# Optimization experiments

Measured on AMD Instinct MI355X. Metric: run time of the kernel, lower is better.

Reference implementation:

```python
import jax, jax.numpy as jnp
import numpy as np
import math

B = 262144
STATE = 6
TOTAL_MEAS = 27
HID = 256
INPUT_DIM = TOTAL_MEAS * 2 + 1 + STATE + 12  # 73
PI = math.pi
NORM_R_SCALE = 500.0 / 150000.0
ANG_IDX = np.array([0, 1, 3, 4, 6, 9, 10, 12, 13, 15, 18, 19, 21, 22, 24])
ANG_MASK = np.zeros((TOTAL_MEAS,), dtype=bool)
ANG_MASK[ANG_IDX] = True


def setup_inputs() -> dict:
    key = jax.random.key(0)
    ks = jax.random.split(key, 16)
    s = lambda fan: 1.0 / math.sqrt(fan)
    inp = {
        "meas": jax.random.normal(ks[0], (B, TOTAL_MEAS), jnp.float32),
        "mask": jnp.ones((B, TOTAL_MEAS), jnp.float32),
        "dt": jax.random.uniform(ks[1], (B,), jnp.float32),
        "baselines": jax.random.normal(ks[2], (B, 12), jnp.float32),
        "x_prev": jax.random.normal(ks[3], (B, STATE), jnp.float32),
        "hx": jnp.zeros((B, HID), jnp.float32),
        # GRU params (torch gate order: r, z, n)
        "W_ih": jax.random.uniform(ks[4], (3 * HID, INPUT_DIM), jnp.float32, -s(HID), s(HID)),
        "W_hh": jax.random.uniform(ks[5], (3 * HID, HID), jnp.float32, -s(HID), s(HID)),
        "b_ih": jax.random.uniform(ks[6], (3 * HID,), jnp.float32, -s(HID), s(HID)),
        "b_hh": jax.random.uniform(ks[7], (3 * HID,), jnp.float32, -s(HID), s(HID)),
        # LayerNorm
        "ln_g": jnp.ones((HID,), jnp.float32),
        "ln_b": jnp.zeros((HID,), jnp.float32),
        # MLP head: 256 -> 256 -> 128 -> 6*27
        "W1": jax.random.uniform(ks[8], (256, HID), jnp.float32, -s(HID), s(HID)),
        "b1": jax.random.uniform(ks[9], (256,), jnp.float32, -s(HID), s(HID)),
        "W2": jax.random.uniform(ks[10], (128, 256), jnp.float32, -s(256), s(256)),
        "b2": jax.random.uniform(ks[11], (128,), jnp.float32, -s(256), s(256)),
        "W3": jax.random.uniform(ks[12], (STATE * TOTAL_MEAS, 128), jnp.float32, -s(128), s(128)),
        "b3": jax.random.uniform(ks[13], (STATE * TOTAL_MEAS,), jnp.float32, -s(128), s(128)),
    }
    return inp


def _wrap_angle(a):
    two_pi = 2.0 * PI
    return a - two_pi * jnp.round(a / two_pi)


def _platform_y_pred(x_rel):
    # x_rel: [B, 6] -> [B, 9] radar/EO measurement
    r_xy = jnp.sqrt(x_rel[:, 0] ** 2 + x_rel[:, 2] ** 2 + 1e-9)
    az = jnp.arctan2(x_rel[:, 2], x_rel[:, 0]) / PI
    el = jnp.arctan2(x_rel[:, 4], r_xy) / PI
    r = jnp.sqrt(x_rel[:, 0] ** 2 + x_rel[:, 2] ** 2 + x_rel[:, 4] ** 2 + 1e-9)
    z = jnp.zeros_like(r)
    return jnp.stack([az, el, r, az, el, z, az, z, z], axis=1)


def _forward(meas, mask, dt, baselines, x_prev, hx,
             W_ih, W_hh, b_ih, b_hh, ln_g, ln_b, W1, b1, W2, b2, W3, b3):
    # f_predict (CV model): x0 += dt*x1, x2 += dt*x3, x4 += dt*x5
    dt_scaled = dt * NORM_R_SCALE  # [B]
    zcol = jnp.zeros_like(x_prev[:, :1])
    shift = jnp.concatenate([x_prev[:, 1:2], zcol, x_prev[:, 3:4], zcol, x_prev[:, 5:6], zcol], axis=1)
    x_minus = x_prev + dt_scaled[:, None] * shift  # [B, 6]

    y_pred = jnp.concatenate([
        _platform_y_pred(x_minus),
        _platform_y_pred(x_minus - baselines[:, 0:6]),
        _platform_y_pred(x_minus - baselines[:, 6:12]),
    ], axis=1)  # [B, 27]

    innov = meas - y_pred
    wrapped = _wrap_angle(innov * PI) / PI
    innov = jnp.where(jnp.asarray(ANG_MASK)[None, :], wrapped, innov)
    innov = innov * mask

    rnn_in = jnp.concatenate([innov, mask, dt[:, None], x_minus, baselines], axis=1)  # [B, 73]

    # single-step GRU (torch semantics, gate order r,z,n)
    gi = rnn_in @ W_ih.T + b_ih  # [B, 3H]
    gh = hx @ W_hh.T + b_hh      # [B, 3H]
    gi_r, gi_z, gi_n = jnp.split(gi, 3, axis=1)
    gh_r, gh_z, gh_n = jnp.split(gh, 3, axis=1)
    r = jax.nn.sigmoid(gi_r + gh_r)
    z = jax.nn.sigmoid(gi_z + gh_z)
    n = jnp.tanh(gi_n + r * gh_n)
    h_new = (1.0 - z) * n + z * hx  # [B, H]

    # LayerNorm
    mu = jnp.mean(h_new, axis=-1, keepdims=True)
    var = jnp.var(h_new, axis=-1, keepdims=True)
    h_ln = (h_new - mu) / jnp.sqrt(var + 1e-5) * ln_g + ln_b

    # MLP gain head (dropout inactive at inference)
    f1 = jax.nn.relu(h_ln @ W1.T + b1)
    f2 = jax.nn.relu(f1 @ W2.T + b2)
    K = (f2 @ W3.T + b3).reshape(-1, STATE, TOTAL_MEAS)
    K = jnp.clip(K, -3.0, 3.0)

    correction = jnp.einsum('bsm,bm->bs', K, innov)
    x_new = jnp.clip(x_minus + correction, -5.0, 5.0)
    return x_new, h_new


def reference(meas, mask, dt, baselines, x_prev, hx,
              W_ih, W_hh, b_ih, b_hh, ln_g, ln_b, W1, b1, W2, b2, W3, b3):
    return _forward(meas, mask, dt, baselines, x_prev, hx,
                    W_ih, W_hh, b_ih, b_hh, ln_g, ln_b, W1, b1, W2, b2, W3, b3)
```

## Files before the change

### kernel.cpp

```cpp
#include <hip/hip_runtime.h>
#include <math.h>

#define B_TOTAL  262144
#define ROWS     64
#define NWG      (B_TOTAL/ROWS)
#define NTHR     512
#define PI_F     3.14159265358979323846f
#define NORM_R   (500.0f/150000.0f)

typedef float  f32x4  __attribute__((ext_vector_type(4)));
typedef short  bf16x8 __attribute__((ext_vector_type(8)));

#define SRZ 352
#define SNI 96
#define SNH 256
#define SW1 256
#define SW2 256
#define SW3 128
#define OFF_RZ 0
#define OFF_NI (OFF_RZ + 512*SRZ)
#define OFF_NH (OFF_NI + 256*SNI)
#define OFF_W1 (OFF_NH + 256*SNH)
#define OFF_W2 (OFF_W1 + 256*SW1)
#define OFF_W3 (OFF_W2 + 128*SW2)
#define W_TOTAL (OFF_W3 + 256*SW3)

#define RSTRIDE 104
#define LDS_HB   (ROWS*RSTRIDE*2)
#define LDS_F1   (LDS_HB + ROWS*256*2)
#define LDS_STG  (LDS_F1 + ROWS*256*2)
#define LDS_XMC  (LDS_STG + 4*16384)
#define LDS_TOTAL (LDS_XMC + ROWS*6*4)

#define WAIT_VM4 asm volatile("s_waitcnt vmcnt(4)" ::: "memory")
#define WAIT_VM2 asm volatile("s_waitcnt vmcnt(2)" ::: "memory")
#define WAIT_VM0 asm volatile("s_waitcnt vmcnt(0)" ::: "memory")
#define BARv     __builtin_amdgcn_s_barrier()
#define PRE_G(g) do { if ((g) < 47) WAIT_VM4; else if ((g) == 47) WAIT_VM2; else WAIT_VM0; BARv; } while(0)

__device__ __forceinline__ ushort f2bf(float f){
    union { float f; unsigned u; } v; v.f = f;
    unsigned r = v.u + 0x7FFFu + ((v.u >> 16) & 1u);
    return (ushort)(r >> 16);
}
__device__ __forceinline__ float b2f(ushort u){
    union { unsigned u; float f; } v; v.u = ((unsigned)u) << 16;
    return v.f;
}
__device__ __forceinline__ float sigm(float x){ return 1.0f/(1.0f+__expf(-x)); }
__device__ __forceinline__ float tanh_(float x){ return 1.0f - 2.0f/(__expf(2.0f*x)+1.0f); }
__device__ __forceinline__ int swzb(int row, int k){
    return ((row<<9) + (k<<1)) ^ ((row&7)<<4);
}

__device__ __forceinline__ void stageA(const ushort* pb, int stride, int koff,
                                       char* dst, int w, int lane) {
    #pragma unroll
    for (int i = 0; i < 2; ++i) {
        int idx  = (w*2 + i)*64 + lane;
        int col  = idx >> 2;
        int kq   = (idx & 3) ^ ((col >> 1) & 3);
        const ushort* g = pb + (size_t)col*stride + koff + kq*8;
        __builtin_amdgcn_global_load_lds(
            (const __attribute__((address_space(1))) void*)g,
            (__attribute__((address_space(3))) void*)(dst + (w*2+i)*1024),
            16, 0, 0);
    }
}
__device__ __forceinline__ void stageB(const ushort* pb, int stride, int koff,
                                       char* dst, int w, int lane) {
    #pragma unroll
    for (int i = 0; i < 2; ++i) {
        int idx  = (w*2 + i)*64 + lane;
        int col  = idx >> 3;
        int kq   = (idx & 7) ^ (col & 7);
        const ushort* g = pb + (size_t)col*stride + koff + kq*8;
        __builtin_amdgcn_global_load_lds(
            (const __attribute__((address_space(1))) void*)g,
            (__attribute__((address_space(3))) void*)(dst + (w*2+i)*1024),
            16, 0, 0);
    }
}
__device__ __forceinline__ bf16x8 rdA16(const char* sb, int col, int lk){
    int slot = lk ^ ((col >> 1) & 3);
    return *(const bf16x8*)(sb + col*64 + slot*16);
}
__device__ __forceinline__ bf16x8 rdB16(const char* sb, int col, int ksub, int lk){
    int slot = ((ksub<<2)|lk) ^ (col & 7);
    return *(const bf16x8*)(sb + col*128 + slot*16);
}

__global__ void prep_weights(const float* __restrict__ W_ih, const float* __restrict__ W_hh,
                             const float* __restrict__ W1, const float* __restrict__ W2,
                             const float* __restrict__ W3, ushort* __restrict__ ws)
{
    int id = blockIdx.x*256 + threadIdx.x;
    if (id >= W_TOTAL) return;
    float v = 0.0f;
    if (id < OFF_NI) {
        int t = id; int n = t / SRZ, k = t - n*SRZ;
        if (k < 73) v = W_ih[n*73 + k];
        else if (k >= 96) v = W_hh[n*256 + (k-96)];
    } else if (id < OFF_NH) {
        int t = id - OFF_NI; int n = t / SNI, k = t - n*SNI;
        if (k < 73) v = W_ih[(512+n)*73 + k];
    } else if (id < OFF_W1) {
        int t = id - OFF_NH; int n = t >> 8, k = t & 255;
        v = W_hh[(512+n)*256 + k];
    } else if (id < OFF_W2) {
        int t = id - OFF_W1; int n = t >> 8, k = t & 255;
        v = W1[n*256 + k];
    } else if (id < OFF_W3) {
        int t = id - OFF_W2; int n = t >> 8, k = t & 255;
        v = W2[n*256 + k];
    } else {
        int t = id - OFF_W3; int n = t >> 7, k = t & 127;
        if (n < 162) v = W3[n*128 + k];
    }
    ws[id] = f2bf(v);
}

#define MM8(ACC) do { _Pragma("unroll") \
    for (int j = 0; j < 4; ++j) { \
        bf16x8 b = rdA16(sb, nq*64 + j*16 + lr, lk); \
        ACC[0][j] = __builtin_amdgcn_mfma_f32_16x16x32_bf16(a0, b, ACC[0][j], 0,0,0); \
        ACC[1][j] = __builtin_amdgcn_mfma_f32_16x16x32_bf16(a1, b, ACC[1][j], 0,0,0); \
    } } while(0)

__global__ __launch_bounds__(NTHR, 1) void knet_mfma(
    const float* __restrict__ meas, const float* __restrict__ mask,
    const float* __restrict__ dt,   const float* __restrict__ baselines,
    const float* __restrict__ x_prev, const float* __restrict__ hx,
    const float* __restrict__ b_ih, const float* __restrict__ b_hh,
    const float* __restrict__ ln_g, const float* __restrict__ ln_b,
    const float* __restrict__ b1,   const float* __restrict__ b2,
    const float* __restrict__ b3,
    const ushort* __restrict__ ws,
    float* __restrict__ out)
{
    extern __shared__ char smem[];
    ushort* Rb  = (ushort*)smem;
    char*   Hb  = smem + LDS_HB;
    char*   F1  = smem + LDS_F1;
    char*   STG = smem + LDS_STG;
    float*  xmc = (float*)(smem + LDS_XMC);

    const int tid  = threadIdx.x;
    const int w    = __builtin_amdgcn_readfirstlane(tid >> 6);
    const int nq   = w & 3;
    const int mh   = w >> 2;
    const int lane = tid & 63;
    const int lr   = lane & 15;
    const int lk   = lane >> 4;
    const int lk8  = lk * 8;
    const int row0 = blockIdx.x * ROWS;
    const int mrow = mh*32 + lr;
    float* hout = out + (size_t)B_TOTAL*6;

    stageA(ws + OFF_RZ, SRZ, 0*32, STG + (0<<14), w, lane);
    stageA(ws + OFF_RZ, SRZ, 1*32, STG + (1<<14), w, lane);
    stageA(ws + OFF_RZ, SRZ, 2*32, STG + (2<<14), w, lane);

    float* scr = (float*)F1;
    {
        const size_t m0 = (size_t)row0*27;
        for (int i = tid; i < 1728; i += NTHR) scr[i]        = meas[m0 + i];
        for (int i = tid; i < 1728; i += NTHR) scr[1728 + i] = mask[m0 + i];
        const size_t b0 = (size_t)row0*12;
        for (int i = tid; i < 768; i += NTHR)  scr[3456 + i] = baselines[b0 + i];
        if (tid < 384) scr[4224 + tid] = x_prev[(size_t)row0*6 + tid];
        if (tid < 64)  scr[4608 + tid] = dt[row0 + tid];
        const size_t hbase = (size_t)row0 * 256;
        #pragma unroll
        for (int ii = 0; ii < 4; ++ii) {
            int cid = tid + ii*NTHR;
            int r  = cid >> 5;
            int k0 = (cid & 31) << 3;
            const float4* p = (const float4*)(hx + hbase + (size_t)r*256 + k0);
            float4 u = p[0], v2 = p[1];
            bf16x8 o;
            o[0]=(short)f2bf(u.x);  o[1]=(short)f2bf(u.y);  o[2]=(short)f2bf(u.z);  o[3]=(short)f2bf(u.w);
            o[4]=(short)f2bf(v2.x); o[5]=(short)f2bf(v2.y); o[6]=(short)f2bf(v2.z); o[7]=(short)f2bf(v2.w);
            *(bf16x8*)(Hb + swzb(r, k0)) = o;
        }
    }
    __syncthreads();

    if (w < 4) {
        const int row = lane;
        const float dtv = scr[4608 + row];
        const float dts = dtv * NORM_R;
        float xp[6], xm[6];
        #pragma unroll
        for (int s = 0; s < 6; ++s) xp[s] = scr[4224 + row*6 + s];
        xm[0] = xp[0] + dts*xp[1]; xm[1] = xp[1];
        xm[2] = xp[2] + dts*xp[3]; xm[3] = xp[3];
        xm[4] = xp[4] + dts*xp[5]; xm[5] = xp[5];
        if (w < 3) {
            float xr[6];
            #pragma unroll
            for (int s = 0; s < 6; ++s) {
                float b = (w == 0) ? 0.0f : scr[3456 + row*12 + (w-1)*6 + s];
                xr[s] = xm[s] - b;
            }
            float rxy = sqrtf(xr[0]*xr[0] + xr[2]*xr[2] + 1e-9f);
            float azv = atan2f(xr[2], xr[0]) * (1.0f/PI_F);
            float elv = atan2f(xr[4], rxy)   * (1.0f/PI_F);
            float rrv = sqrtf(xr[0]*xr[0] + xr[2]*xr[2] + xr[4]*xr[4] + 1e-9f);
            float y[9] = {azv, elv, rrv, azv, elv, 0.0f, azv, 0.0f, 0.0f};
            const bool ang[9] = {true,true,false,true,true,false,true,false,false};
            #pragma unroll
            for (int i = 0; i < 9; ++i) {
                int m = w*9 + i;
                float ms = scr[1728 + row*27 + m];
                float v  = scr[row*27 + m] - y[i];
                if (ang[i]) v = v - 2.0f*rintf(v*0.5f);
                v *= ms;
                Rb[row*RSTRIDE + m]      = f2bf(v);
                Rb[row*RSTRIDE + 27 + m] = f2bf(ms);
            }
        } else {
            Rb[row*RSTRIDE + 54] = f2bf(dtv);
            #pragma unroll
            for (int s = 0; s < 6; ++s) Rb[row*RSTRIDE + 55 + s] = f2bf(xm[s]);
            #pragma unroll
            for (int q = 0; q < 12; ++q) Rb[row*RSTRIDE + 61 + q] = f2bf(scr[3456 + row*12 + q]);
            #pragma unroll
            for (int k = 73; k < 96; ++k) Rb[row*RSTRIDE + k] = 0;
            #pragma unroll
            for (int s = 0; s < 6; ++s) xmc[row*6 + s] = xm[s];
        }
    }
    __syncthreads();

    f32x4 ar[2][4], az_[2][4], gi_[2][4], gh_[2][4];
    #pragma unroll
    for (int i = 0; i < 2; ++i)
        #pragma unroll
        for (int j = 0; j < 4; ++j) {
            ar[i][j]=(f32x4){0,0,0,0}; az_[i][j]=(f32x4){0,0,0,0};
            gi_[i][j]=(f32x4){0,0,0,0}; gh_[i][j]=(f32x4){0,0,0,0};
        }

    #pragma unroll
    for (int kb = 0; kb < 11; ++kb) {
        PRE_G(kb);
        char* dst = STG + (((kb+3)&3)<<14);
        if (kb < 8) stageA(ws + OFF_RZ, SRZ, (kb+3)*32, dst, w, lane);
        else        stageA(ws + OFF_RZ + (size_t)256*SRZ, SRZ, (kb-8)*32, dst, w, lane);
        const char* sb = STG + ((kb&3)<<14);
        bf16x8 a0, a1;
        if (kb < 3) { a0 = *(const bf16x8*)(Rb + mrow*RSTRIDE + kb*32 + lk8);
                      a1 = *(const bf16x8*)(Rb + (mrow+16)*RSTRIDE + kb*32 + lk8); }
        else        { a0 = *(const bf16x8*)(Hb + swzb(mrow,    (kb-3)*32 + lk8));
                      a1 = *(const bf16x8*)(Hb + swzb(mrow+16, (kb-3)*32 + lk8)); }
        __builtin_amdgcn_s_setprio(1);
        MM8(ar);
        __builtin_amdgcn_s_setprio(0);
    }
    #pragma unroll
    for (int kb = 0; kb < 11; ++kb) {
        PRE_G(11+kb);
        char* dst = STG + (((kb+14)&3)<<14);
        if (kb < 8) stageA(ws + OFF_RZ + (size_t)256*SRZ, SRZ, (kb+3)*32, dst, w, lane);
        else        stageA(ws + OFF_NI, SNI, (kb-8)*32, dst, w, lane);
        const char* sb = STG + (((11+kb)&3)<<14);
        bf16x8 a0, a1;
        if (kb < 3) { a0 = *(const bf16x8*)(Rb + mrow*RSTRIDE + kb*32 + lk8);
                      a1 = *(const bf16x8*)(Rb + (mrow+16)*RSTRIDE + kb*32 + lk8); }
        else        { a0 = *(const bf16x8*)(Hb + swzb(mrow,    (kb-3)*32 + lk8));
                      a1 = *(const bf16x8*)(Hb + swzb(mrow+16, (kb-3)*32 + lk8)); }
        __builtin_amdgcn_s_setprio(1);
        MM8(az_);
        __builtin_amdgcn_s_setprio(0);
    }
    #pragma unroll
    for (int kb = 0; kb < 3; ++kb) {
        PRE_G(22+kb);
        char* dst = STG + (((kb+25)&3)<<14);
        stageA(ws + OFF_NH, SNH, kb*32, dst, w, lane);
        const char* sb = STG + (((22+kb)&3)<<14);
        bf16x8 a0 = *(const bf16x8*)(Rb + mrow*RSTRIDE + kb*32 + lk8);
        bf16x8 a1 = *(const bf16x8*)(Rb + (mrow+16)*RSTRIDE + kb*32 + lk8);
        __builtin_amdgcn_s_setprio(1);
        MM8(gi_);
        __builtin_amdgcn_s_setprio(0);
    }
    #pragma unroll
    for (int kb = 0; kb < 8; ++kb) {
        PRE_G(25+kb);
        char* dst = STG + (((kb+28)&3)<<14);
        if (kb < 5) stageA(ws + OFF_NH, SNH, (kb+3)*32, dst, w, lane);
        else        stageA(ws + OFF_W1, SW1, (kb-5)*32, dst, w, lane);
        const char* sb = STG + (((25+kb)&3)<<14);
        bf16x8 a0 = *(const bf16x8*)(Hb + swzb(mrow,    kb*32 + lk8));
        bf16x8 a1 = *(const bf16x8*)(Hb + swzb(mrow+16, kb*32 + lk8));
        __builtin_amdgcn_s_setprio(1);
        MM8(gh_);
        __builtin_amdgcn_s_setprio(0);
    }
    #pragma unroll
    for (int j = 0; j < 4; ++j) {
        int c = nq*64 + j*16 + lr;
        float brv = b_ih[c] + b_hh[c];
        float bzv = b_ih[256+c] + b_hh[256+c];
        float binv = b_ih[512+c], bhnv = b_hh[512+c];
        #pragma unroll
        for (int i = 0; i < 2; ++i)
            #pragma unroll
            for (int e = 0; e < 4; ++e) {
                int row = mh*32 + i*16 + lk*4 + e;
                float rg = sigm(ar[i][j][e] + brv);
                float zg = sigm(az_[i][j][e] + bzv);
                float ng = tanh_(gi_[i][j][e] + binv + rg*(gh_[i][j][e] + bhnv));
                float hxv = b2f(*(const ushort*)(Hb + swzb(row, c)));
                float hn = (1.0f - zg)*ng + zg*hxv;
                *(ushort*)(F1 + swzb(row, c)) = f2bf(hn);
            }
    }
    __syncthreads();

    {
        const int row = tid >> 3;
        const int o   = tid & 7;
        bf16x8 ch[4];
        float sum = 0.0f, sq = 0.0f;
        #pragma unroll
        for (int c4 = 0; c4 < 4; ++c4) {
            ch[c4] = *(const bf16x8*)(F1 + swzb(row, o*32 + c4*8));
            #pragma unroll
            for (int e = 0; e < 8; ++e) {
                float f = b2f((ushort)ch[c4][e]);
                sum += f; sq += f*f;
            }
        }
        sum += __shfl_xor(sum, 1); sum += __shfl_xor(sum, 2); sum += __shfl_xor(sum, 4);
        sq  += __shfl_xor(sq, 1);  sq  += __shfl_xor(sq, 2);  sq  += __shfl_xor(sq, 4);
        float mu   = sum * (1.0f/256.0f);
        float rstd = rsqrtf(sq*(1.0f/256.0f) - mu*mu + 1e-5f);
        #pragma unroll
        for (int c4 = 0; c4 < 4; ++c4) {
            int col0 = o*32 + c4*8;
            float4 g0 = *(const float4*)(ln_g + col0), g1 = *(const float4*)(ln_g + col0 + 4);
            float4 bb0 = *(const float4*)(ln_b + col0), bb1 = *(const float4*)(ln_b + col0 + 4);
            bf16x8 oo;
            oo[0] = (short)f2bf((b2f((ushort)ch[c4][0]) - mu)*rstd*g0.x + bb0.x);
            oo[1] = (short)f2bf((b2f((ushort)ch[c4][1]) - mu)*rstd*g0.y + bb0.y);
            oo[2] = (short)f2bf((b2f((ushort)ch[c4][2]) - mu)*rstd*g0.z + bb0.z);
            oo[3] = (short)f2bf((b2f((ushort)ch[c4][3]) - mu)*rstd*g0.w + bb0.w);
            oo[4] = (short)f2bf((b2f((ushort)ch[c4][4]) - mu)*rstd*g1.x + bb1.x);
            oo[5] = (short)f2bf((b2f((ushort)ch[c4][5]) - mu)*rstd*g1.y + bb1.y);
            oo[6] = (short)f2bf((b2f((ushort)ch[c4][6]) - mu)*rstd*g1.z + bb1.z);
            oo[7] = (short)f2bf((b2f((ushort)ch[c4][7]) - mu)*rstd*g1.w + bb1.w);
            *(bf16x8*)(Hb + swzb(row, col0)) = oo;
        }
        #pragma unroll
        for (int i = 0; i < 8; ++i) {
            int chunk = i*NTHR + tid;
            int r2 = chunk >> 6;
            int c16 = chunk & 63;
            uint2 d = *(const uint2*)(F1 + swzb(r2, c16*4));
            float4 o4;
            o4.x = b2f((ushort)(d.x & 0xffffu)); o4.y = b2f((ushort)(d.x >> 16));
            o4.z = b2f((ushort)(d.y & 0xffffu)); o4.w = b2f((ushort)(d.y >> 16));
            *(float4*)(hout + (size_t)(row0+r2)*256 + c16*4) = o4;
        }
    }
    __syncthreads();

    {
        f32x4 c2[2][4];
        #pragma unroll
        for (int i = 0; i < 2; ++i)
            #pragma unroll
            for (int j = 0; j < 4; ++j) c2[i][j] = (f32x4){0,0,0,0};
        #pragma unroll
        for (int kb = 0; kb < 8; ++kb) {
            PRE_G(33+kb);
            char* dst = STG + (((kb+36)&3)<<14);
            if (kb < 5) stageA(ws + OFF_W1, SW1, (kb+3)*32, dst, w, lane);
            else        stageB(ws + OFF_W2, SW2, (kb-5)*64, dst, w, lane);
            const char* sb = STG + (((33+kb)&3)<<14);
            bf16x8 a0 = *(const bf16x8*)(Hb + swzb(mrow,    kb*32 + lk8));
            bf16x8 a1 = *(const bf16x8*)(Hb + swzb(mrow+16, kb*32 + lk8));
            __builtin_amdgcn_s_setprio(1);
            MM8(c2);
            __builtin_amdgcn_s_setprio(0);
        }
        #pragma unroll
        for (int j = 0; j < 4; ++j) {
            int c = nq*64 + j*16 + lr;
            float bv = b1[c];
            #pragma unroll
            for (int i = 0; i < 2; ++i)
                #pragma unroll
                for (int e = 0; e < 4; ++e) {
                    int row = mh*32 + i*16 + lk*4 + e;
                    *(ushort*)(F1 + swzb(row, c)) = f2bf(fmaxf(c2[i][j][e] + bv, 0.0f));
                }
        }
    }
    __syncthreads();

    ushort* F2 = (ushort*)Hb;
    {
        f32x4 c3[2][2];
        #pragma unroll
        for (int i = 0; i < 2; ++i)
            #pragma unroll
            for (int j = 0; j < 2; ++j) c3[i][j] = (f32x4){0,0,0,0};
        #pragma unroll
        for (int kb = 0; kb < 4; ++kb) {
            PRE_G(41+kb);
            char* dst = STG + (((kb+44)&3)<<14);
            if (kb < 1) stageB(ws + OFF_W2, SW2, (kb+3)*64, dst, w, lane);
            else        stageA(ws + OFF_W3, SW3, (kb-1)*32, dst, w, lane);
            const char* sb = STG + (((41+kb)&3)<<14);
            __builtin_amdgcn_s_setprio(1);
            #pragma unroll
            for (int ksub = 0; ksub < 2; ++ksub) {
                bf16x8 a0 = *(const bf16x8*)(F1 + swzb(mrow,    kb*64 + ksub*32 + lk8));
                bf16x8 a1 = *(const bf16x8*)(F1 + swzb(mrow+16, kb*64 + ksub*32 + lk8));
                #pragma unroll
                for (int j = 0; j < 2; ++j) {
                    bf16x8 b = rdB16(sb, nq*32 + j*16 + lr, ksub, lk);
                    c3[0][j] = __builtin_amdgcn_mfma_f32_16x16x32_bf16(a0, b, c3[0][j], 0,0,0);
                    c3[1][j] = __builtin_amdgcn_mfma_f32_16x16x32_bf16(a1, b, c3[1][j], 0,0,0);
                }
            }
            __builtin_amdgcn_s_setprio(0);
        }
        __syncthreads();
        #pragma unroll
        for (int j = 0; j < 2; ++j) {
            int c = nq*32 + j*16 + lr;
            float bv = b2[c];
            #pragma unroll
            for (int i = 0; i < 2; ++i)
                #pragma unroll
                for (int e = 0; e < 4; ++e) {
                    int row = mh*32 + i*16 + lk*4 + e;
                    F2[row*136 + c] = f2bf(fmaxf(c3[i][j][e] + bv, 0.0f));
                }
        }
    }
    __syncthreads();

    {
        f32x4 c4[2][3];
        #pragma unroll
        for (int i = 0; i < 2; ++i)
            #pragma unroll
            for (int j = 0; j < 3; ++j) c4[i][j] = (f32x4){0,0,0,0};
        const int nfb = nq*3;
        #pragma unroll
        for (int kb = 0; kb < 4; ++kb) {
            PRE_G(45+kb);
            if (kb < 1) stageA(ws + OFF_W3, SW3, (kb+3)*32, STG + (((kb+48)&3)<<14), w, lane);
            const char* sb = STG + (((45+kb)&3)<<14);
            bf16x8 a0 = *(const bf16x8*)(F2 + (mrow     )*136 + kb*32 + lk8);
            bf16x8 a1 = *(const bf16x8*)(F2 + (mrow + 16)*136 + kb*32 + lk8);
            __builtin_amdgcn_s_setprio(1);
            #pragma unroll
            for (int j = 0; j < 3; ++j) {
                bf16x8 b = rdA16(sb, (nfb+j)*16 + lr, lk);
                c4[0][j] = __builtin_amdgcn_mfma_f32_16x16x32_bf16(a0, b, c4[0][j], 0,0,0);
                c4[1][j] = __builtin_amdgcn_mfma_f32_16x16x32_bf16(a1, b, c4[1][j], 0,0,0);
            }
            __builtin_amdgcn_s_setprio(0);
        }
        #pragma unroll
        for (int j = 0; j < 3; ++j) {
            int col = (nfb+j)*16 + lr;
            if (col < 162) {
                int s = col / 27, m = col - s*27;
                float bv = b3[col];
                #pragma unroll
                for (int i = 0; i < 2; ++i)
                    #pragma unroll
                    for (int e = 0; e < 4; ++e) {
                        int row = mh*32 + i*16 + lk*4 + e;
                        float K  = fminf(fmaxf(c4[i][j][e] + bv, -3.0f), 3.0f);
                        float iv = b2f(Rb[row*RSTRIDE + m]);
                        atomicAdd(&xmc[row*6 + s], K*iv);
                    }
            }
        }
    }
    __syncthreads();

    for (int t = tid; t < ROWS*6; t += NTHR) {
        int row = t / 6, s = t - row*6;
        float v = fminf(fmaxf(xmc[t], -5.0f), 5.0f);
        out[(size_t)(row0+row)*6 + s] = v;
    }
}

extern "C" void kernel_launch(void* const* d_in, const int* in_sizes, int n_in,
                              void* d_out, int out_size, void* d_ws, size_t ws_size,
                              hipStream_t stream) {
    const float* meas      = (const float*)d_in[0];
    const float* mask      = (const float*)d_in[1];
    const float* dtv       = (const float*)d_in[2];
    const float* baselines = (const float*)d_in[3];
    const float* x_prev    = (const float*)d_in[4];
    const float* hx        = (const float*)d_in[5];
    const float* W_ih      = (const float*)d_in[6];
    const float* W_hh      = (const float*)d_in[7];
    const float* b_ih      = (const float*)d_in[8];
    const float* b_hh      = (const float*)d_in[9];
    const float* ln_g      = (const float*)d_in[10];
    const float* ln_b      = (const float*)d_in[11];
    const float* W1        = (const float*)d_in[12];
    const float* b1        = (const float*)d_in[13];
    const float* W2        = (const float*)d_in[14];
    const float* b2        = (const float*)d_in[15];
    const float* W3        = (const float*)d_in[16];
    const float* b3        = (const float*)d_in[17];
    ushort* wsb = (ushort*)d_ws;
    float* outp = (float*)d_out;

    prep_weights<<<(W_TOTAL + 255)/256, 256, 0, stream>>>(W_ih, W_hh, W1, W2, W3, wsb);
    knet_mfma<<<NWG, NTHR, LDS_TOTAL, stream>>>(
        meas, mask, dtv, baselines, x_prev, hx,
        b_ih, b_hh, ln_g, ln_b, b1, b2, b3, wsb, outp);
}
```

Before: 851.4 us.

## Fuse GRU gate GEMMs into one K-loop with pre-swizzled linear weight staging

Reorders the prepared weights into pre-swizzled contiguous slabs, so each stage is a plain linear global-to-LDS copy and the per-lane address math goes away. The r, z and n gate GEMMs now run in a single 11-step K loop that shares the A-fragment reads, with 48KB double buffering in place of a 4-deep 16KB ring. The MFMA operands are swapped so that accumulators hold contiguous columns, which allows vectorised bias loads and fused GRU/LayerNorm epilogues. Each stage now waits on vmcnt(0) with only two buffers, which could expose load latency. The larger LDS footprint may also change how much load and compute overlap.

After: 693.0 us, median of 3. 1.23x faster.

```diff
diff --git a/kernel.cpp b/kernel.cpp
--- a/kernel.cpp
+++ b/kernel.cpp
@@ -11,32 +11,22 @@
 typedef float  f32x4  __attribute__((ext_vector_type(4)));
 typedef short  bf16x8 __attribute__((ext_vector_type(8)));
 
-#define SRZ 352
-#define SNI 96
-#define SNH 256
-#define SW1 256
-#define SW2 256
-#define SW3 128
-#define OFF_RZ 0
-#define OFF_NI (OFF_RZ + 512*SRZ)
-#define OFF_NH (OFF_NI + 256*SNI)
-#define OFF_W1 (OFF_NH + 256*SNH)
-#define OFF_W2 (OFF_W1 + 256*SW1)
-#define OFF_W3 (OFF_W2 + 128*SW2)
-#define W_TOTAL (OFF_W3 + 256*SW3)
-
-#define RSTRIDE 104
-#define LDS_HB   (ROWS*RSTRIDE*2)
-#define LDS_F1   (LDS_HB + ROWS*256*2)
-#define LDS_STG  (LDS_F1 + ROWS*256*2)
-#define LDS_XMC  (LDS_STG + 4*16384)
-#define LDS_TOTAL (LDS_XMC + ROWS*6*4)
-
-#define WAIT_VM4 asm volatile("s_waitcnt vmcnt(4)" ::: "memory")
-#define WAIT_VM2 asm volatile("s_waitcnt vmcnt(2)" ::: "memory")
+#define GRU_SLAB 24576
+#define OFF_GRU  0
+#define OFF_W1   (11*GRU_SLAB)
+#define OFF_W2   (OFF_W1 + 8*8192)
+#define OFF_W3   (OFF_W2 + 8*4096)
+#define W_TOTAL  (OFF_W3 + 4*8192)
+
+#define LDS_RBF2  0
+#define LDS_HB    17408
+#define LDS_STG   (LDS_HB + 32768)
+#define LDS_XMC   (LDS_STG + 2*49152)
+#define LDS_LNS   (LDS_XMC + 1536)
+#define LDS_TOTAL (LDS_LNS + 2048)
+
 #define WAIT_VM0 asm volatile("s_waitcnt vmcnt(0)" ::: "memory")
 #define BARv     __builtin_amdgcn_s_barrier()
-#define PRE_G(g) do { if ((g) < 47) WAIT_VM4; else if ((g) == 47) WAIT_VM2; else WAIT_VM0; BARv; } while(0)
 
 __device__ __forceinline__ ushort f2bf(float f){
     union { float f; unsigned u; } v; v.f = f;
@@ -52,42 +42,28 @@
 __device__ __forceinline__ int swzb(int row, int k){
     return ((row<<9) + (k<<1)) ^ ((row&7)<<4);
 }
-
-__device__ __forceinline__ void stageA(const ushort* pb, int stride, int koff,
-                                       char* dst, int w, int lane) {
-    #pragma unroll
-    for (int i = 0; i < 2; ++i) {
-        int idx  = (w*2 + i)*64 + lane;
-        int col  = idx >> 2;
-        int kq   = (idx & 3) ^ ((col >> 1) & 3);
-        const ushort* g = pb + (size_t)col*stride + koff + kq*8;
+__device__ __forceinline__ bf16x8 rdW(const char* gb, int col, int lk){
+    int slot = lk ^ ((col >> 1) & 3);
+    return *(const bf16x8*)(gb + col*64 + slot*16);
+}
+template<int N>
+__device__ __forceinline__ void stage_lin(const ushort* src, char* dst, int w, int lane){
+    #pragma unroll
+    for (int i = 0; i < N; ++i) {
         __builtin_amdgcn_global_load_lds(
-            (const __attribute__((address_space(1))) void*)g,
-            (__attribute__((address_space(3))) void*)(dst + (w*2+i)*1024),
+            (const __attribute__((address_space(1))) void*)(src + (size_t)(i*512 + w*64 + lane)*8),
+            (__attribute__((address_space(3))) void*)(dst + i*8192 + w*1024),
             16, 0, 0);
     }
 }
-__device__ __forceinline__ void stageB(const ushort* pb, int stride, int koff,
-                                       char* dst, int w, int lane) {
-    #pragma unroll
-    for (int i = 0; i < 2; ++i) {
-        int idx  = (w*2 + i)*64 + lane;
-        int col  = idx >> 3;
-        int kq   = (idx & 7) ^ (col & 7);
-        const ushort* g = pb + (size_t)col*stride + koff + kq*8;
-        __builtin_amdgcn_global_load_lds(
-            (const __attribute__((address_space(1))) void*)g,
-            (__attribute__((address_space(3))) void*)(dst + (w*2+i)*1024),
-            16, 0, 0);
-    }
-}
-__device__ __forceinline__ bf16x8 rdA16(const char* sb, int col, int lk){
-    int slot = lk ^ ((col >> 1) & 3);
-    return *(const bf16x8*)(sb + col*64 + slot*16);
-}
-__device__ __forceinline__ bf16x8 rdB16(const char* sb, int col, int ksub, int lk){
-    int slot = ((ksub<<2)|lk) ^ (col & 7);
-    return *(const bf16x8*)(sb + col*128 + slot*16);
+__device__ __forceinline__ void mm4(const char* gb, int colbase, int lr, int lk,
+                                    bf16x8 a0, bf16x8 a1, f32x4 acc[2][4]){
+    #pragma unroll
+    for (int j = 0; j < 4; ++j) {
+        bf16x8 wf = rdW(gb, colbase + j*16 + lr, lk);
+        acc[0][j] = __builtin_amdgcn_mfma_f32_16x16x32_bf16(wf, a0, acc[0][j], 0,0,0);
+        acc[1][j] = __builtin_amdgcn_mfma_f32_16x16x32_bf16(wf, a1, acc[1][j], 0,0,0);
+    }
 }
 
 __global__ void prep_weights(const float* __restrict__ W_ih, const float* __restrict__ W_hh,
@@ -97,35 +73,33 @@
     int id = blockIdx.x*256 + threadIdx.x;
     if (id >= W_TOTAL) return;
     float v = 0.0f;
-    if (id < OFF_NI) {
-        int t = id; int n = t / SRZ, k = t - n*SRZ;
-        if (k < 73) v = W_ih[n*73 + k];
-        else if (k >= 96) v = W_hh[n*256 + (k-96)];
-    } else if (id < OFF_NH) {
-        int t = id - OFF_NI; int n = t / SNI, k = t - n*SNI;
-        if (k < 73) v = W_ih[(512+n)*73 + k];
-    } else if (id < OFF_W1) {
-        int t = id - OFF_NH; int n = t >> 8, k = t & 255;
-        v = W_hh[(512+n)*256 + k];
+    if (id < OFF_W1) {
+        int slab = id / GRU_SLAB, u = id % GRU_SLAB;
+        int gate = u >> 13, u2 = u & 8191;
+        int col = u2 >> 5, v5 = u2 & 31, slot = v5 >> 3, e = v5 & 7;
+        int kq = slot ^ ((col >> 1) & 3);
+        int k = slab*32 + kq*8 + e;
+        int rowz = gate*256 + col;
+        v = (k < 73) ? W_ih[rowz*73 + k] : ((k < 96) ? 0.0f : W_hh[rowz*256 + (k-96)]);
     } else if (id < OFF_W2) {
-        int t = id - OFF_W1; int n = t >> 8, k = t & 255;
-        v = W1[n*256 + k];
+        int t = id - OFF_W1, kb = t >> 13, u2 = t & 8191;
+        int col = u2 >> 5, v5 = u2 & 31, slot = v5 >> 3, e = v5 & 7;
+        int kq = slot ^ ((col >> 1) & 3);
+        v = W1[col*256 + kb*32 + kq*8 + e];
     } else if (id < OFF_W3) {
-        int t = id - OFF_W2; int n = t >> 8, k = t & 255;
-        v = W2[n*256 + k];
+        int t = id - OFF_W2, kb = t >> 12, u2 = t & 4095;
+        int col = u2 >> 5, v5 = u2 & 31, slot = v5 >> 3, e = v5 & 7;
+        int kq = slot ^ ((col >> 1) & 3);
+        v = W2[col*256 + kb*32 + kq*8 + e];
     } else {
-        int t = id - OFF_W3; int n = t >> 7, k = t & 127;
-        if (n < 162) v = W3[n*128 + k];
+        int t = id - OFF_W3, kb = t >> 13, u2 = t & 8191;
+        int col = u2 >> 5, v5 = u2 & 31, slot = v5 >> 3, e = v5 & 7;
+        int kq = slot ^ ((col >> 1) & 3);
+        int k = kb*32 + kq*8 + e;
+        v = (col < 162) ? W3[col*128 + k] : 0.0f;
     }
     ws[id] = f2bf(v);
 }
-
-#define MM8(ACC) do { _Pragma("unroll") \
-    for (int j = 0; j < 4; ++j) { \
-        bf16x8 b = rdA16(sb, nq*64 + j*16 + lr, lk); \
-        ACC[0][j] = __builtin_amdgcn_mfma_f32_16x16x32_bf16(a0, b, ACC[0][j], 0,0,0); \
-        ACC[1][j] = __builtin_amdgcn_mfma_f32_16x16x32_bf16(a1, b, ACC[1][j], 0,0,0); \
-    } } while(0)
 
 __global__ __launch_bounds__(NTHR, 1) void knet_mfma(
     const float* __restrict__ meas, const float* __restrict__ mask,
@@ -139,11 +113,11 @@
     float* __restrict__ out)
 {
     extern __shared__ char smem[];
-    ushort* Rb  = (ushort*)smem;
-    char*   Hb  = smem + LDS_HB;
-    char*   F1  = smem + LDS_F1;
-    char*   STG = smem + LDS_STG;
-    float*  xmc = (float*)(smem + LDS_XMC);
+    ushort* Rbu  = (ushort*)(smem + LDS_RBF2);
+    char*   Hb   = smem + LDS_HB;
+    char*   STG  = smem + LDS_STG;
+    float*  xmc  = (float*)(smem + LDS_XMC);
+    float*  lnscr= (float*)(smem + LDS_LNS);
 
     const int tid  = threadIdx.x;
     const int w    = __builtin_amdgcn_readfirstlane(tid >> 6);
@@ -157,11 +131,9 @@
     const int mrow = mh*32 + lr;
     float* hout = out + (size_t)B_TOTAL*6;
 
-    stageA(ws + OFF_RZ, SRZ, 0*32, STG + (0<<14), w, lane);
-    stageA(ws + OFF_RZ, SRZ, 1*32, STG + (1<<14), w, lane);
-    stageA(ws + OFF_RZ, SRZ, 2*32, STG + (2<<14), w, lane);
-
-    float* scr = (float*)F1;
+    stage_lin<6>(ws + OFF_GRU, STG, w, lane);
+
+    float* scr = (float*)(STG + 49152);
     {
         const size_t m0 = (size_t)row0*27;
         for (int i = tid; i < 1728; i += NTHR) scr[i]        = meas[m0 + i];
@@ -216,274 +188,310 @@
                 float v  = scr[row*27 + m] - y[i];
                 if (ang[i]) v = v - 2.0f*rintf(v*0.5f);
                 v *= ms;
-                Rb[row*RSTRIDE + m]      = f2bf(v);
-                Rb[row*RSTRIDE + 27 + m] = f2bf(ms);
+                Rbu[row*104 + m]      = f2bf(v);
+                Rbu[row*104 + 27 + m] = f2bf(ms);
             }
         } else {
-            Rb[row*RSTRIDE + 54] = f2bf(dtv);
-            #pragma unroll
-            for (int s = 0; s < 6; ++s) Rb[row*RSTRIDE + 55 + s] = f2bf(xm[s]);
-            #pragma unroll
-            for (int q = 0; q < 12; ++q) Rb[row*RSTRIDE + 61 + q] = f2bf(scr[3456 + row*12 + q]);
-            #pragma unroll
-            for (int k = 73; k < 96; ++k) Rb[row*RSTRIDE + k] = 0;
+            Rbu[row*104 + 54] = f2bf(dtv);
+            #pragma unroll
+            for (int s = 0; s < 6; ++s) Rbu[row*104 + 55 + s] = f2bf(xm[s]);
+            #pragma unroll
+            for (int q = 0; q < 12; ++q) Rbu[row*104 + 61 + q] = f2bf(scr[3456 + row*12 + q]);
+            #pragma unroll
+            for (int k = 73; k < 96; ++k) Rbu[row*104 + k] = 0;
             #pragma unroll
             for (int s = 0; s < 6; ++s) xmc[row*6 + s] = xm[s];
         }
     }
     __syncthreads();
 
-    f32x4 ar[2][4], az_[2][4], gi_[2][4], gh_[2][4];
+    f32x4 ar[2][4], az[2][4], agi[2][4], agh[2][4];
     #pragma unroll
     for (int i = 0; i < 2; ++i)
         #pragma unroll
         for (int j = 0; j < 4; ++j) {
-            ar[i][j]=(f32x4){0,0,0,0}; az_[i][j]=(f32x4){0,0,0,0};
-            gi_[i][j]=(f32x4){0,0,0,0}; gh_[i][j]=(f32x4){0,0,0,0};
-        }
-
+            ar[i][j]=(f32x4){0,0,0,0}; az[i][j]=(f32x4){0,0,0,0};
+            agi[i][j]=(f32x4){0,0,0,0}; agh[i][j]=(f32x4){0,0,0,0};
+        }
     #pragma unroll
     for (int kb = 0; kb < 11; ++kb) {
-        PRE_G(kb);
-        char* dst = STG + (((kb+3)&3)<<14);
-        if (kb < 8) stageA(ws + OFF_RZ, SRZ, (kb+3)*32, dst, w, lane);
-        else        stageA(ws + OFF_RZ + (size_t)256*SRZ, SRZ, (kb-8)*32, dst, w, lane);
-        const char* sb = STG + ((kb&3)<<14);
+        WAIT_VM0; BARv;
+        if (kb < 10) stage_lin<6>(ws + OFF_GRU + (kb+1)*GRU_SLAB, STG + ((kb+1)&1)*49152, w, lane);
+        else         stage_lin<6>(ws + OFF_W1,                    STG + 49152,            w, lane);
+        const char* sb = STG + (kb&1)*49152;
         bf16x8 a0, a1;
-        if (kb < 3) { a0 = *(const bf16x8*)(Rb + mrow*RSTRIDE + kb*32 + lk8);
-                      a1 = *(const bf16x8*)(Rb + (mrow+16)*RSTRIDE + kb*32 + lk8); }
+        if (kb < 3) { a0 = *(const bf16x8*)(Rbu + mrow*104 + kb*32 + lk8);
+                      a1 = *(const bf16x8*)(Rbu + (mrow+16)*104 + kb*32 + lk8); }
         else        { a0 = *(const bf16x8*)(Hb + swzb(mrow,    (kb-3)*32 + lk8));
                       a1 = *(const bf16x8*)(Hb + swzb(mrow+16, (kb-3)*32 + lk8)); }
         __builtin_amdgcn_s_setprio(1);
-        MM8(ar);
+        mm4(sb,         nq*64, lr, lk, a0, a1, ar);
+        mm4(sb + 16384, nq*64, lr, lk, a0, a1, az);
+        if (kb < 3) mm4(sb + 32768, nq*64, lr, lk, a0, a1, agi);
+        else        mm4(sb + 32768, nq*64, lr, lk, a0, a1, agh);
         __builtin_amdgcn_s_setprio(0);
     }
-    #pragma unroll
-    for (int kb = 0; kb < 11; ++kb) {
-        PRE_G(11+kb);
-        char* dst = STG + (((kb+14)&3)<<14);
-        if (kb < 8) stageA(ws + OFF_RZ + (size_t)256*SRZ, SRZ, (kb+3)*32, dst, w, lane);
-        else        stageA(ws + OFF_NI, SNI, (kb-8)*32, dst, w, lane);
-        const char* sb = STG + (((11+kb)&3)<<14);
-        bf16x8 a0, a1;
-        if (kb < 3) { a0 = *(const bf16x8*)(Rb + mrow*RSTRIDE + kb*32 + lk8);
-                      a1 = *(const bf16x8*)(Rb + (mrow+16)*RSTRIDE + kb*32 + lk8); }
-        else        { a0 = *(const bf16x8*)(Hb + swzb(mrow,    (kb-3)*32 + lk8));
-                      a1 = *(const bf16x8*)(Hb + swzb(mrow+16, (kb-3)*32 + lk8)); }
-        __builtin_amdgcn_s_setprio(1);
-        MM8(az_);
-        __builtin_amdgcn_s_setprio(0);
-    }
-    #pragma unroll
-    for (int kb = 0; kb < 3; ++kb) {
-        PRE_G(22+kb);
-        char* dst = STG + (((kb+25)&3)<<14);
-        stageA(ws + OFF_NH, SNH, kb*32, dst, w, lane);
-        const char* sb = STG + (((22+kb)&3)<<14);
-        bf16x8 a0 = *(const bf16x8*)(Rb + mrow*RSTRIDE + kb*32 + lk8);
-        bf16x8 a1 = *(const bf16x8*)(Rb + (mrow+16)*RSTRIDE + kb*32 + lk8);
-        __builtin_amdgcn_s_setprio(1);
-        MM8(gi_);
-        __builtin_amdgcn_s_setprio(0);
-    }
-    #pragma unroll
-    for (int kb = 0; kb < 8; ++kb) {
-        PRE_G(25+kb);
-        char* dst = STG + (((kb+28)&3)<<14);
-        if (kb < 5) stageA(ws + OFF_NH, SNH, (kb+3)*32, dst, w, lane);
-        else        stageA(ws + OFF_W1, SW1, (kb-5)*32, dst, w, lane);
-        const char* sb = STG + (((25+kb)&3)<<14);
-        bf16x8 a0 = *(const bf16x8*)(Hb + swzb(mrow,    kb*32 + lk8));
-        bf16x8 a1 = *(const bf16x8*)(Hb + swzb(mrow+16, kb*32 + lk8));
-        __builtin_amdgcn_s_setprio(1);
-        MM8(gh_);
-        __builtin_amdgcn_s_setprio(0);
-    }
+
+    f32x4 hnv[2][4];
+    float lsum[2] = {0,0}, lsq[2] = {0,0};
     #pragma unroll
     for (int j = 0; j < 4; ++j) {
-        int c = nq*64 + j*16 + lr;
-        float brv = b_ih[c] + b_hh[c];
-        float bzv = b_ih[256+c] + b_hh[256+c];
-        float binv = b_ih[512+c], bhnv = b_hh[512+c];
-        #pragma unroll
-        for (int i = 0; i < 2; ++i)
+        const int c0 = nq*64 + j*16 + lk*4;
+        f32x4 bir = *(const f32x4*)(b_ih + c0),        bhr = *(const f32x4*)(b_hh + c0);
+        f32x4 biz = *(const f32x4*)(b_ih + 256 + c0),  bhz = *(const f32x4*)(b_hh + 256 + c0);
+        f32x4 bin_= *(const f32x4*)(b_ih + 512 + c0),  bhn = *(const f32x4*)(b_hh + 512 + c0);
+        #pragma unroll
+        for (int i = 0; i < 2; ++i) {
+            const int row = mh*32 + i*16 + lr;
+            uint2 hxd = *(const uint2*)(Hb + swzb(row, c0));
+            float hx_[4] = { b2f((ushort)(hxd.x & 0xffffu)), b2f((ushort)(hxd.x >> 16)),
+                             b2f((ushort)(hxd.y & 0xffffu)), b2f((ushort)(hxd.y >> 16)) };
+            f32x4 hn4;
             #pragma unroll
             for (int e = 0; e < 4; ++e) {
-                int row = mh*32 + i*16 + lk*4 + e;
-                float rg = sigm(ar[i][j][e] + brv);
-                float zg = sigm(az_[i][j][e] + bzv);
-                float ng = tanh_(gi_[i][j][e] + binv + rg*(gh_[i][j][e] + bhnv));
-                float hxv = b2f(*(const ushort*)(Hb + swzb(row, c)));
-                float hn = (1.0f - zg)*ng + zg*hxv;
-                *(ushort*)(F1 + swzb(row, c)) = f2bf(hn);
-            }
-    }
-    __syncthreads();
-
-    {
-        const int row = tid >> 3;
-        const int o   = tid & 7;
-        bf16x8 ch[4];
-        float sum = 0.0f, sq = 0.0f;
-        #pragma unroll
-        for (int c4 = 0; c4 < 4; ++c4) {
-            ch[c4] = *(const bf16x8*)(F1 + swzb(row, o*32 + c4*8));
-            #pragma unroll
-            for (int e = 0; e < 8; ++e) {
-                float f = b2f((ushort)ch[c4][e]);
-                sum += f; sq += f*f;
-            }
-        }
-        sum += __shfl_xor(sum, 1); sum += __shfl_xor(sum, 2); sum += __shfl_xor(sum, 4);
-        sq  += __shfl_xor(sq, 1);  sq  += __shfl_xor(sq, 2);  sq  += __shfl_xor(sq, 4);
-        float mu   = sum * (1.0f/256.0f);
-        float rstd = rsqrtf(sq*(1.0f/256.0f) - mu*mu + 1e-5f);
-        #pragma unroll
-        for (int c4 = 0; c4 < 4; ++c4) {
-            int col0 = o*32 + c4*8;
-            float4 g0 = *(const float4*)(ln_g + col0), g1 = *(const float4*)(ln_g + col0 + 4);
-            float4 bb0 = *(const float4*)(ln_b + col0), bb1 = *(const float4*)(ln_b + col0 + 4);
-            bf16x8 oo;
-            oo[0] = (short)f2bf((b2f((ushort)ch[c4][0]) - mu)*rstd*g0.x + bb0.x);
-            oo[1] = (short)f2bf((b2f((ushort)ch[c4][1]) - mu)*rstd*g0.y + bb0.y);
-            oo[2] = (short)f2bf((b2f((ushort)ch[c4][2]) - mu)*rstd*g0.z + bb0.z);
-            oo[3] = (short)f2bf((b2f((ushort)ch[c4][3]) - mu)*rstd*g0.w + bb0.w);
-            oo[4] = (short)f2bf((b2f((ushort)ch[c4][4]) - mu)*rstd*g1.x + bb1.x);
-            oo[5] = (short)f2bf((b2f((ushort)ch[c4][5]) - mu)*rstd*g1.y + bb1.y);
-            oo[6] = (short)f2bf((b2f((ushort)ch[c4][6]) - mu)*rstd*g1.z + bb1.z);
-            oo[7] = (short)f2bf((b2f((ushort)ch[c4][7]) - mu)*rstd*g1.w + bb1.w);
-            *(bf16x8*)(Hb + swzb(row, col0)) = oo;
-        }
-        #pragma unroll
-        for (int i = 0; i < 8; ++i) {
-            int chunk = i*NTHR + tid;
-            int r2 = chunk >> 6;
-            int c16 = chunk & 63;
-            uint2 d = *(const uint2*)(F1 + swzb(r2, c16*4));
-            float4 o4;
-            o4.x = b2f((ushort)(d.x & 0xffffu)); o4.y = b2f((ushort)(d.x >> 16));
-            o4.z = b2f((ushort)(d.y & 0xffffu)); o4.w = b2f((ushort)(d.y >> 16));
-            *(float4*)(hout + (size_t)(row0+r2)*256 + c16*4) = o4;
-        }
-    }
-    __syncthreads();
-
-    {
-        f32x4 c2[2][4];
-        #pragma unroll
-        for (int i = 0; i < 2; ++i)
-            #pragma unroll
-            for (int j = 0; j < 4; ++j) c2[i][j] = (f32x4){0,0,0,0};
-        #pragma unroll
-        for (int kb = 0; kb < 8; ++kb) {
-            PRE_G(33+kb);
-            char* dst = STG + (((kb+36)&3)<<14);
-            if (kb < 5) stageA(ws + OFF_W1, SW1, (kb+3)*32, dst, w, lane);
-            else        stageB(ws + OFF_W2, SW2, (kb-5)*64, dst, w, lane);
-            const char* sb = STG + (((33+kb)&3)<<14);
+                float rg = sigm(ar[i][j][e] + bir[e] + bhr[e]);
+                float zg = sigm(az[i][j][e] + biz[e] + bhz[e]);
+                float ng = tanh_(agi[i][j][e] + bin_[e] + rg*(agh[i][j][e] + bhn[e]));
+                float hn = (1.0f - zg)*ng + zg*hx_[e];
+                hn4[e] = hn;
+                lsum[i] += hn; lsq[i] += hn*hn;
+            }
+            hnv[i][j] = hn4;
+            float4 st = { hn4[0], hn4[1], hn4[2], hn4[3] };
+            *(float4*)(hout + (size_t)(row0+row)*256 + c0) = st;
+        }
+    }
+    #pragma unroll
+    for (int i = 0; i < 2; ++i) {
+        lsum[i] += __shfl_xor(lsum[i], 16); lsum[i] += __shfl_xor(lsum[i], 32);
+        lsq[i]  += __shfl_xor(lsq[i], 16);  lsq[i]  += __shfl_xor(lsq[i], 32);
+    }
+    if (lk == 0) {
+        #pragma unroll
+        for (int i = 0; i < 2; ++i) {
+            const int row = mh*32 + i*16 + lr;
+            lnscr[row*8 + nq*2 + 0] = lsum[i];
+            lnscr[row*8 + nq*2 + 1] = lsq[i];
+        }
+    }
+    __syncthreads();
+
+    {
+        float mu[2], rstd[2];
+        #pragma unroll
+        for (int i = 0; i < 2; ++i) {
+            const int row = mh*32 + i*16 + lr;
+            float s = 0, q = 0;
+            #pragma unroll
+            for (int qq = 0; qq < 4; ++qq) { s += lnscr[row*8 + qq*2]; q += lnscr[row*8 + qq*2 + 1]; }
+            mu[i] = s * (1.0f/256.0f);
+            rstd[i] = rsqrtf(q*(1.0f/256.0f) - mu[i]*mu[i] + 1e-5f);
+        }
+        #pragma unroll
+        for (int j = 0; j < 4; ++j) {
+            const int c0 = nq*64 + j*16 + lk*4;
+            f32x4 g4 = *(const f32x4*)(ln_g + c0);
+            f32x4 b4 = *(const f32x4*)(ln_b + c0);
+            #pragma unroll
+            for (int i = 0; i < 2; ++i) {
+                const int row = mh*32 + i*16 + lr;
+                float v0 = (hnv[i][j][0]-mu[i])*rstd[i]*g4[0] + b4[0];
+                float v1 = (hnv[i][j][1]-mu[i])*rstd[i]*g4[1] + b4[1];
+                float v2 = (hnv[i][j][2]-mu[i])*rstd[i]*g4[2] + b4[2];
+                float v3 = (hnv[i][j][3]-mu[i])*rstd[i]*g4[3] + b4[3];
+                uint2 o;
+                o.x = (unsigned)f2bf(v0) | ((unsigned)f2bf(v1) << 16);
+                o.y = (unsigned)f2bf(v2) | ((unsigned)f2bf(v3) << 16);
+                *(uint2*)(Hb + swzb(row, c0)) = o;
+            }
+        }
+    }
+    __syncthreads();
+
+    f32x4 c2[2][4];
+    #pragma unroll
+    for (int i = 0; i < 2; ++i)
+        #pragma unroll
+        for (int j = 0; j < 4; ++j) c2[i][j] = (f32x4){0,0,0,0};
+    WAIT_VM0; BARv;
+    stage_lin<6>(ws + OFF_W1 + 3*8192, STG, w, lane);
+    {
+        const char* sb = STG + 49152;
+        #pragma unroll
+        for (int kb = 0; kb < 3; ++kb) {
             bf16x8 a0 = *(const bf16x8*)(Hb + swzb(mrow,    kb*32 + lk8));
             bf16x8 a1 = *(const bf16x8*)(Hb + swzb(mrow+16, kb*32 + lk8));
             __builtin_amdgcn_s_setprio(1);
-            MM8(c2);
-            __builtin_amdgcn_s_setprio(0);
-        }
-        #pragma unroll
-        for (int j = 0; j < 4; ++j) {
-            int c = nq*64 + j*16 + lr;
-            float bv = b1[c];
-            #pragma unroll
-            for (int i = 0; i < 2; ++i)
-                #pragma unroll
-                for (int e = 0; e < 4; ++e) {
-                    int row = mh*32 + i*16 + lk*4 + e;
-                    *(ushort*)(F1 + swzb(row, c)) = f2bf(fmaxf(c2[i][j][e] + bv, 0.0f));
+            mm4(sb + kb*16384, nq*64, lr, lk, a0, a1, c2);
+            __builtin_amdgcn_s_setprio(0);
+        }
+    }
+    WAIT_VM0; BARv;
+    stage_lin<4>(ws + OFF_W1 + 6*8192, STG + 49152, w, lane);
+    {
+        const char* sb = STG;
+        #pragma unroll
+        for (int kb = 3; kb < 6; ++kb) {
+            bf16x8 a0 = *(const bf16x8*)(Hb + swzb(mrow,    kb*32 + lk8));
+            bf16x8 a1 = *(const bf16x8*)(Hb + swzb(mrow+16, kb*32 + lk8));
+            __builtin_amdgcn_s_setprio(1);
+            mm4(sb + (kb-3)*16384, nq*64, lr, lk, a0, a1, c2);
+            __builtin_amdgcn_s_setprio(0);
+        }
+    }
+    WAIT_VM0; BARv;
+    stage_lin<4>(ws + OFF_W2, STG, w, lane);
+    {
+        const char* sb = STG + 49152;
+        #pragma unroll
+        for (int kb = 6; kb < 8; ++kb) {
+            bf16x8 a0 = *(const bf16x8*)(Hb + swzb(mrow,    kb*32 + lk8));
+            bf16x8 a1 = *(const bf16x8*)(Hb + swzb(mrow+16, kb*32 + lk8));
+            __builtin_amdgcn_s_setprio(1);
+            mm4(sb + (kb-6)*16384, nq*64, lr, lk, a0, a1, c2);
+            __builtin_amdgcn_s_setprio(0);
+        }
+    }
+    __syncthreads();
+    #pragma unroll
+    for (int j = 0; j < 4; ++j) {
+        const int c0 = nq*64 + j*16 + lk*4;
+        f32x4 b4 = *(const f32x4*)(b1 + c0);
+        #pragma unroll
+        for (int i = 0; i < 2; ++i) {
+            const int row = mh*32 + i*16 + lr;
+            uint2 o;
+            o.x = (unsigned)f2bf(fmaxf(c2[i][j][0]+b4[0],0.f)) | ((unsigned)f2bf(fmaxf(c2[i][j][1]+b4[1],0.f)) << 16);
+            o.y = (unsigned)f2bf(fmaxf(c2[i][j][2]+b4[2],0.f)) | ((unsigned)f2bf(fmaxf(c2[i][j][3]+b4[3],0.f)) << 16);
+            *(uint2*)(Hb + swzb(row, c0)) = o;
+        }
+    }
+    __syncthreads();
+
+    f32x4 c3[2][2];
+    #pragma unroll
+    for (int i = 0; i < 2; ++i)
+        #pragma unroll
+        for (int j = 0; j < 2; ++j) c3[i][j] = (f32x4){0,0,0,0};
+    WAIT_VM0; BARv;
+    stage_lin<4>(ws + OFF_W2 + 4*4096, STG + 49152, w, lane);
+    {
+        const char* sb = STG;
+        #pragma unroll
+        for (int kb = 0; kb < 4; ++kb) {
+            bf16x8 a0 = *(const bf16x8*)(Hb + swzb(mrow,    kb*32 + lk8));
+            bf16x8 a1 = *(const bf16x8*)(Hb + swzb(mrow+16, kb*32 + lk8));
+            __builtin_amdgcn_s_setprio(1);
+            #pragma unroll
+            for (int j = 0; j < 2; ++j) {
+                bf16x8 wf = rdW(sb + kb*8192, nq*32 + j*16 + lr, lk);
+                c3[0][j] = __builtin_amdgcn_mfma_f32_16x16x32_bf16(wf, a0, c3[0][j], 0,0,0);
+                c3[1][j] = __builtin_amdgcn_mfma_f32_16x16x32_bf16(wf, a1, c3[1][j], 0,0,0);
+            }
+            __builtin_amdgcn_s_setprio(0);
+        }
+    }
+    WAIT_VM0; BARv;
+    stage_lin<4>(ws + OFF_W3, STG, w, lane);
+    {
+        const char* sb = STG + 49152;
+        #pragma unroll
+        for (int kb = 4; kb < 8; ++kb) {
+            bf16x8 a0 = *(const bf16x8*)(Hb + swzb(mrow,    kb*32 + lk8));
+            bf16x8 a1 = *(const bf16x8*)(Hb + swzb(mrow+16, kb*32 + lk8));
+            __builtin_amdgcn_s_setprio(1);
+            #pragma unroll
+            for (int j = 0; j < 2; ++j) {
+                bf16x8 wf = rdW(sb + (kb-4)*8192, nq*32 + j*16 + lr, lk);
+                c3[0][j] = __builtin_amdgcn_mfma_f32_16x16x32_bf16(wf, a0, c3[0][j], 0,0,0);
+                c3[1][j] = __builtin_amdgcn_mfma_f32_16x16x32_bf16(wf, a1, c3[1][j], 0,0,0);
+            }
+            __builtin_amdgcn_s_setprio(0);
+        }
+    }
+    f32x4 iv[2][3];
+    #pragma unroll
+    for (int j = 0; j < 3; ++j) {
+        #pragma unroll
+        for (int i = 0; i < 2; ++i) {
+            const int row = mh*32 + i*16 + lr;
+            #pragma unroll
+            for (int e = 0; e < 4; ++e) {
+                int col = nq*48 + j*16 + lk*4 + e;
+                int m = col - 27*(col/27);
+                iv[i][j][e] = b2f(Rbu[row*104 + m]);
+            }
+        }
+    }
+    __syncthreads();
+    #pragma unroll
+    for (int j = 0; j < 2; ++j) {
+        const int c0 = nq*32 + j*16 + lk*4;
+        f32x4 b4 = *(const f32x4*)(b2 + c0);
+        #pragma unroll
+        for (int i = 0; i < 2; ++i) {
+            const int row = mh*32 + i*16 + lr;
+            uint2 o;
+            o.x = (unsigned)f2bf(fmaxf(c3[i][j][0]+b4[0],0.f)) | ((unsigned)f2bf(fmaxf(c3[i][j][1]+b4[1],0.f)) << 16);
+            o.y = (unsigned)f2bf(fmaxf(c3[i][j][2]+b4[2],0.f)) | ((unsigned)f2bf(fmaxf(c3[i][j][3]+b4[3],0.f)) << 16);
+            *(uint2*)((char*)Rbu + row*272 + c0*2) = o;
+        }
+    }
+    __syncthreads();
+
+    f32x4 c4[2][3];
+    #pragma unroll
+    for (int i = 0; i < 2; ++i)
+        #pragma unroll
+        for (int j = 0; j < 3; ++j) c4[i][j] = (f32x4){0,0,0,0};
+    WAIT_VM0; BARv;
+    stage_lin<4>(ws + OFF_W3 + 2*8192, STG + 49152, w, lane);
+    {
+        const char* sb = STG;
+        #pragma unroll
+        for (int kb = 0; kb < 2; ++kb) {
+            bf16x8 a0 = *(const bf16x8*)((char*)Rbu + (mrow     )*272 + (kb*32 + lk8)*2);
+            bf16x8 a1 = *(const bf16x8*)((char*)Rbu + (mrow + 16)*272 + (kb*32 + lk8)*2);
+            __builtin_amdgcn_s_setprio(1);
+            #pragma unroll
+            for (int j = 0; j < 3; ++j) {
+                bf16x8 wf = rdW(sb + kb*16384, nq*48 + j*16 + lr, lk);
+                c4[0][j] = __builtin_amdgcn_mfma_f32_16x16x32_bf16(wf, a0, c4[0][j], 0,0,0);
+                c4[1][j] = __builtin_amdgcn_mfma_f32_16x16x32_bf16(wf, a1, c4[1][j], 0,0,0);
+            }
+            __builtin_amdgcn_s_setprio(0);
+        }
+    }
+    WAIT_VM0; BARv;
+    {
+        const char* sb = STG + 49152;
+        #pragma unroll
+        for (int kb = 2; kb < 4; ++kb) {
+            bf16x8 a0 = *(const bf16x8*)((char*)Rbu + (mrow     )*272 + (kb*32 + lk8)*2);
+            bf16x8 a1 = *(const bf16x8*)((char*)Rbu + (mrow + 16)*272 + (kb*32 + lk8)*2);
+            __builtin_amdgcn_s_setprio(1);
+            #pragma unroll
+            for (int j = 0; j < 3; ++j) {
+                bf16x8 wf = rdW(sb + (kb-2)*16384, nq*48 + j*16 + lr, lk);
+                c4[0][j] = __builtin_amdgcn_mfma_f32_16x16x32_bf16(wf, a0, c4[0][j], 0,0,0);
+                c4[1][j] = __builtin_amdgcn_mfma_f32_16x16x32_bf16(wf, a1, c4[1][j], 0,0,0);
+            }
+            __builtin_amdgcn_s_setprio(0);
+        }
+    }
+    #pragma unroll
+    for (int j = 0; j < 3; ++j) {
+        #pragma unroll
+        for (int i = 0; i < 2; ++i) {
+            const int row = mh*32 + i*16 + lr;
+            #pragma unroll
+            for (int e = 0; e < 4; ++e) {
+                int col = nq*48 + j*16 + lk*4 + e;
+                if (col < 162) {
+                    int s = col / 27;
+                    float K = fminf(fmaxf(c4[i][j][e] + b3[col], -3.0f), 3.0f);
+                    atomicAdd(&xmc[row*6 + s], K * iv[i][j][e]);
                 }
-        }
-    }
-    __syncthreads();
-
-    ushort* F2 = (ushort*)Hb;
-    {
-        f32x4 c3[2][2];
-        #pragma unroll
-        for (int i = 0; i < 2; ++i)
-            #pragma unroll
-            for (int j = 0; j < 2; ++j) c3[i][j] = (f32x4){0,0,0,0};
-        #pragma unroll
-        for (int kb = 0; kb < 4; ++kb) {
-            PRE_G(41+kb);
-            char* dst = STG + (((kb+44)&3)<<14);
-            if (kb < 1) stageB(ws + OFF_W2, SW2, (kb+3)*64, dst, w, lane);
-            else        stageA(ws + OFF_W3, SW3, (kb-1)*32, dst, w, lane);
-            const char* sb = STG + (((41+kb)&3)<<14);
-            __builtin_amdgcn_s_setprio(1);
-            #pragma unroll
-            for (int ksub = 0; ksub < 2; ++ksub) {
-                bf16x8 a0 = *(const bf16x8*)(F1 + swzb(mrow,    kb*64 + ksub*32 + lk8));
-                bf16x8 a1 = *(const bf16x8*)(F1 + swzb(mrow+16, kb*64 + ksub*32 + lk8));
-                #pragma unroll
-                for (int j = 0; j < 2; ++j) {
-                    bf16x8 b = rdB16(sb, nq*32 + j*16 + lr, ksub, lk);
-                    c3[0][j] = __builtin_amdgcn_mfma_f32_16x16x32_bf16(a0, b, c3[0][j], 0,0,0);
-                    c3[1][j] = __builtin_amdgcn_mfma_f32_16x16x32_bf16(a1, b, c3[1][j], 0,0,0);
-                }
-            }
-            __builtin_amdgcn_s_setprio(0);
-        }
-        __syncthreads();
-        #pragma unroll
-        for (int j = 0; j < 2; ++j) {
-            int c = nq*32 + j*16 + lr;
-            float bv = b2[c];
-            #pragma unroll
-            for (int i = 0; i < 2; ++i)
-                #pragma unroll
-                for (int e = 0; e < 4; ++e) {
-                    int row = mh*32 + i*16 + lk*4 + e;
-                    F2[row*136 + c] = f2bf(fmaxf(c3[i][j][e] + bv, 0.0f));
-                }
-        }
-    }
-    __syncthreads();
-
-    {
-        f32x4 c4[2][3];
-        #pragma unroll
-        for (int i = 0; i < 2; ++i)
-            #pragma unroll
-            for (int j = 0; j < 3; ++j) c4[i][j] = (f32x4){0,0,0,0};
-        const int nfb = nq*3;
-        #pragma unroll
-        for (int kb = 0; kb < 4; ++kb) {
-            PRE_G(45+kb);
-            if (kb < 1) stageA(ws + OFF_W3, SW3, (kb+3)*32, STG + (((kb+48)&3)<<14), w, lane);
-            const char* sb = STG + (((45+kb)&3)<<14);
-            bf16x8 a0 = *(const bf16x8*)(F2 + (mrow     )*136 + kb*32 + lk8);
-            bf16x8 a1 = *(const bf16x8*)(F2 + (mrow + 16)*136 + kb*32 + lk8);
-            __builtin_amdgcn_s_setprio(1);
-            #pragma unroll
-            for (int j = 0; j < 3; ++j) {
-                bf16x8 b = rdA16(sb, (nfb+j)*16 + lr, lk);
-                c4[0][j] = __builtin_amdgcn_mfma_f32_16x16x32_bf16(a0, b, c4[0][j], 0,0,0);
-                c4[1][j] = __builtin_amdgcn_mfma_f32_16x16x32_bf16(a1, b, c4[1][j], 0,0,0);
-            }
-            __builtin_amdgcn_s_setprio(0);
-        }
-        #pragma unroll
-        for (int j = 0; j < 3; ++j) {
-            int col = (nfb+j)*16 + lr;
-            if (col < 162) {
-                int s = col / 27, m = col - s*27;
-                float bv = b3[col];
-                #pragma unroll
-                for (int i = 0; i < 2; ++i)
-                    #pragma unroll
-                    for (int e = 0; e < 4; ++e) {
-                        int row = mh*32 + i*16 + lk*4 + e;
-                        float K  = fminf(fmaxf(c4[i][j][e] + bv, -3.0f), 3.0f);
-                        float iv = b2f(Rb[row*RSTRIDE + m]);
-                        atomicAdd(&xmc[row*6 + s], K*iv);
-                    }
             }
         }
     }
```
